# Optimization experiments

Measured on AMD Instinct MI355X. Metric: run time of the kernel, lower is better.

## Reference

```python
import jax, jax.numpy as jnp
import numpy as np
from jax import lax

B, N, D, L, EDGE_H, NGNN = 8, 128, 256, 64, 64, 3


def setup_inputs() -> dict:
    key = jax.random.key(0)
    ks = iter(jax.random.split(key, 64))
    def nrm(shape, s=0.02):
        return jax.random.normal(next(ks), shape, jnp.float32) * s
    inp = {}
    inp["node_feats"] = jax.random.uniform(next(ks), (B, N, 11), jnp.float32)
    inp["edge_feats"] = jax.random.normal(next(ks), (B, N, N, 3), jnp.float32)
    inp["adj_mask"] = jax.random.randint(next(ks), (B, N, N), 0, 2).astype(bool)
    inp["layer_costs"] = jax.random.uniform(next(ks), (B, L), jnp.float32)
    inp["global_dynamic"] = jax.random.uniform(next(ks), (B, 2), jnp.float32)
    inp["p_node_w"] = nrm((11, D)); inp["p_node_b"] = jnp.zeros((D,), jnp.float32)
    inp["g_w1"] = nrm((NGNN, D + 3, EDGE_H)); inp["g_b1"] = jnp.zeros((NGNN, EDGE_H), jnp.float32)
    inp["g_w2"] = nrm((NGNN, EDGE_H, D)); inp["g_b2"] = jnp.zeros((NGNN, D), jnp.float32)
    inp["u_w1"] = nrm((NGNN, 3 * D, D)); inp["u_b1"] = jnp.zeros((NGNN, D), jnp.float32)
    inp["u_w2"] = nrm((NGNN, D, D)); inp["u_b2"] = jnp.zeros((NGNN, D), jnp.float32)
    inp["ln_g"] = jnp.ones((NGNN, D), jnp.float32); inp["ln_b"] = jnp.zeros((NGNN, D), jnp.float32)
    inp["conv_w"] = nrm((32, 1, 4)); inp["conv_b"] = jnp.zeros((32,), jnp.float32)
    inp["lp_w"] = nrm((32 * 31, D)); inp["lp_b"] = jnp.zeros((D,), jnp.float32)
    inp["q_w"] = nrm((2 * D + 2, D)); inp["q_b"] = jnp.zeros((D,), jnp.float32)
    inp["k_w"] = nrm((D, D)); inp["k_b"] = jnp.zeros((D,), jnp.float32)
    inp["s_w1"] = nrm((D + 2, D)); inp["s_b1"] = jnp.zeros((D,), jnp.float32)
    inp["s_w2"] = nrm((D, 1)); inp["s_b2"] = jnp.zeros((1,), jnp.float32)
    inp["v_w1"] = nrm((2 * D + 2, D)); inp["v_b1"] = jnp.zeros((D,), jnp.float32)
    inp["v_w2"] = nrm((D, 1)); inp["v_b2"] = jnp.zeros((1,), jnp.float32)
    return inp


def _ecgc(h, edge_feats, adj_bool, gw1, gb1, gw2, gb2, uw1, ub1, uw2, ub2, lng, lnb):
    Bh, Nn, Dd = h.shape
    # h_j: features of sender node j broadcast over receiver axis -> (B, N, N, D)
    h_j = jnp.broadcast_to(h[:, None, :, :], (Bh, Nn, Nn, Dd))
    gate_in = jnp.concatenate([h_j, edge_feats], axis=-1)            # (B,N,N,D+3)
    gates = jax.nn.sigmoid(jax.nn.relu(gate_in @ gw1 + gb1) @ gw2 + gb2)
    msg = gates * h_j                                                # (B,N,N,D)
    m = adj_bool.astype(h.dtype)[..., None]
    cnt = jnp.maximum(m.sum(axis=2), 1.0)                            # (B,N,1)
    agg_mean = (msg * m).sum(axis=2) / cnt                           # (B,N,D)
    agg_max = jnp.where(adj_bool[..., None], msg, -jnp.inf).max(axis=2)
    agg_max = jnp.where(jnp.isinf(agg_max), 0.0, agg_max)
    ui = jnp.concatenate([h, agg_mean, agg_max], axis=-1)            # (B,N,3D)
    x = h + (jax.nn.relu(ui @ uw1 + ub1) @ uw2 + ub2)
    mu = x.mean(-1, keepdims=True)
    var = ((x - mu) ** 2).mean(-1, keepdims=True)
    return (x - mu) * lax.rsqrt(var + 1e-5) * lng + lnb


def reference(node_feats, edge_feats, adj_mask, layer_costs, global_dynamic,
              p_node_w, p_node_b, g_w1, g_b1, g_w2, g_b2, u_w1, u_b1, u_w2, u_b2,
              ln_g, ln_b, conv_w, conv_b, lp_w, lp_b, q_w, q_b, k_w, k_b,
              s_w1, s_b1, s_w2, s_b2, v_w1, v_b1, v_w2, v_b2):
    # layer cost encoder: Conv1d(1,32,k=4,s=2) + ReLU, flatten, Linear
    le = lax.conv_general_dilated(layer_costs[:, None, :], conv_w, (2,), 'VALID',
                                  dimension_numbers=('NCH', 'OIH', 'NCH'))
    le = jax.nn.relu(le + conv_b[None, :, None])                     # (B,32,31)
    layer_embed = le.reshape(le.shape[0], -1) @ lp_w + lp_b          # (B,D)
    h = node_feats @ p_node_w + p_node_b                             # (B,N,D)
    for i in range(g_w1.shape[0]):
        h = _ecgc(h, edge_feats, adj_mask, g_w1[i], g_b1[i], g_w2[i], g_b2[i],
                  u_w1[i], u_b1[i], u_w2[i], u_b2[i], ln_g[i], ln_b[i])
    w = (node_feats[:, :, 0] * node_feats[:, :, 7])[..., None]       # (B,N,1)
    graph_embed = (w * h).sum(axis=1) / jnp.maximum(w.sum(axis=1), 1e-8)
    qi = jnp.concatenate([graph_embed, layer_embed, global_dynamic], axis=-1)
    query = qi @ q_w + q_b                                           # (B,D)
    keys = h @ k_w + k_b                                             # (B,N,D)
    device_scores = jnp.einsum('bnd,bd->bn', keys, query) / jnp.sqrt(jnp.float32(query.shape[-1]))
    si = jnp.concatenate([graph_embed, global_dynamic], axis=-1)
    stop_logit = jax.nn.relu(si @ s_w1 + s_b1) @ s_w2 + s_b2         # (B,1)
    all_logits = jnp.concatenate([device_scores, stop_logit], axis=1)
    value = jax.nn.relu(qi @ v_w1 + v_b1) @ v_w2 + v_b2              # (B,1)
    return all_logits, value, h
```

## Files before the change

### kernel.cpp

```cpp
#include <hip/hip_runtime.h>
#include <hip/hip_bf16.h>
#include <math.h>

#define BB 8
#define NN_ 128
#define DD 256
#define LL 64
#define EH 64
#define NG 3

typedef __attribute__((ext_vector_type(8))) short bs8;
typedef __attribute__((ext_vector_type(4))) float f4;

__device__ __forceinline__ short f2bf(float f) {
    __hip_bfloat16 h = __float2bfloat16(f);
    return *reinterpret_cast<short*>(&h);
}

__device__ __forceinline__ bs8 cvt8(const float* __restrict__ p) {
    bs8 r;
    #pragma unroll
    for (int i = 0; i < 8; ++i) r[i] = f2bf(p[i]);
    return r;
}

__device__ __forceinline__ float blockReduceSum(float v, float* sRed) {
    int tid = threadIdx.x;
    __syncthreads();
    sRed[tid] = v;
    __syncthreads();
    for (int s = 128; s > 0; s >>= 1) {
        if (tid < s) sRed[tid] += sRed[tid + s];
        __syncthreads();
    }
    return sRed[0];
}

__global__ __launch_bounds__(256) void k_prep(
    const float* __restrict__ uw1, const float* __restrict__ uw2,
    const float* __restrict__ gw2, const float* __restrict__ gw1,
    const float* __restrict__ kw, const unsigned char* __restrict__ adj,
    const float* __restrict__ lc, const float* __restrict__ cw,
    const float* __restrict__ cb, const float* __restrict__ lpw,
    const float* __restrict__ nf, const float* __restrict__ pnw,
    const float* __restrict__ pnb, const float* __restrict__ gb1,
    unsigned short* __restrict__ w1t, unsigned short* __restrict__ w2t,
    unsigned short* __restrict__ g2t, unsigned short* __restrict__ g1t,
    unsigned short* __restrict__ kwt, int* __restrict__ mode,
    float* __restrict__ lpart, float* __restrict__ wsum,
    float* __restrict__ h, float* __restrict__ preg)
{
    const int blk = blockIdx.x, tid = threadIdx.x;
    if (blk == 232) {
        __shared__ int sOff, sBig;
        __shared__ float sRedD[256];
        if (tid == 0) { sOff = 0; sBig = 0; }
        __syncthreads();
        int off = 0, big = 0;
        #pragma unroll
        for (int k = 0; k < 4; ++k) {
            unsigned char v = adj[tid * 4 + k];
            if (v > 1) big = 1;
            if (k != 0 && v != 0) off = 1;
        }
        if (off) atomicOr(&sOff, 1);
        if (big) atomicOr(&sBig, 1);
        __syncthreads();
        if (tid == 0) mode[0] = sBig ? 2 : (sOff ? 0 : 1);
        for (int bb = 0; bb < 8; ++bb) {
            float v = 0.f;
            if (tid < 128) {
                const float* p = nf + (size_t)(bb * 128 + tid) * 11;
                v = p[0] * p[7];
            }
            float s = blockReduceSum(v, sRedD);
            if (tid == 0) wsum[bb] = s;
        }
        return;
    }
    if (blk >= 489) {
        const int row0 = (blk - 489) * 16;
        __shared__ float sF[16][12];
        __shared__ float sCW[12][64];
        if (tid < 176) sF[tid / 11][tid % 11] = nf[(size_t)(row0 + tid / 11) * 11 + tid % 11];
        {
            const int t = tid & 63, f0 = tid >> 6;
            const float* r0p = pnw + (size_t)f0 * DD;
            const float* r1p = pnw + (size_t)(f0 + 4) * DD;
            const float* r2p = (f0 + 8 < 11) ? (pnw + (size_t)(f0 + 8) * DD) : pnb;
            float a0 = 0.f, a1 = 0.f, a2 = 0.f;
            for (int k = 0; k < 256; ++k) {
                float g = gw1[k * EH + t];
                a0 += r0p[k] * g; a1 += r1p[k] * g; a2 += r2p[k] * g;
            }
            if (f0 + 8 == 11) a2 += gb1[t];
            sCW[f0][t] = a0; sCW[f0 + 4][t] = a1; sCW[f0 + 8][t] = a2;
        }
        __syncthreads();
        float acc[16];
        {
            float bb = pnb[tid];
            #pragma unroll
            for (int rr = 0; rr < 16; ++rr) acc[rr] = bb;
        }
        #pragma unroll
        for (int f = 0; f < 11; ++f) {
            float wf = pnw[f * DD + tid];
            #pragma unroll
            for (int rr = 0; rr < 16; ++rr) acc[rr] += sF[rr][f] * wf;
        }
        #pragma unroll
        for (int rr = 0; rr < 16; ++rr)
            h[(size_t)(row0 + rr) * DD + tid] = acc[rr];
        {
            const int t = tid & 63, r0 = tid >> 6;
            #pragma unroll
            for (int q = 0; q < 4; ++q) {
                int rr = r0 * 4 + q;
                float a = sCW[11][t];
                #pragma unroll
                for (int f = 0; f < 11; ++f) a += sF[rr][f] * sCW[f][t];
                preg[(size_t)(row0 + rr) * EH + t] = a;
            }
        }
        return;
    }
    if (blk > 232) {
        const int lb = blk - 233;
        const int b = lb >> 5, kseg = (lb >> 2) & 7, c4 = lb & 3;
        const int d = tid & 63, ss = tid >> 6;
        __shared__ float sC[LL];
        __shared__ float sV[124];
        __shared__ float sP[4][64];
        if (tid < LL) sC[tid] = lc[b * LL + tid];
        __syncthreads();
        if (tid < 124) {
            int idx = kseg * 124 + tid;
            int c = idx / 31, t = idx - c * 31;
            float a = cb[c];
            #pragma unroll
            for (int k = 0; k < 4; ++k) a += sC[2 * t + k] * cw[c * 4 + k];
            sV[tid] = fmaxf(a, 0.f);
        }
        __syncthreads();
        float acc = 0.f;
        for (int k = ss; k < 124; k += 4)
            acc += sV[k] * lpw[(size_t)(kseg * 124 + k) * DD + c4 * 64 + d];
        sP[ss][d] = acc;
        __syncthreads();
        if (ss == 0)
            lpart[(b * 32 + kseg * 4 + c4) * 64 + d] = sP[0][d] + sP[1][d] + sP[2][d] + sP[3][d];
        return;
    }
    const float* src; unsigned short* dst; int K, kt, dt, srcw = 256;
    if (blk < 144)      { int l = blk / 48, t = blk % 48; kt = t >> 2; dt = t & 3;
                          src = uw1 + (size_t)l * 196608; dst = w1t + (size_t)l * 196608; K = 768; }
    else if (blk < 192) { int x = blk - 144, l = x / 16, t = x % 16; kt = t >> 2; dt = t & 3;
                          src = uw2 + (size_t)l * 65536; dst = w2t + (size_t)l * 65536; K = 256; }
    else if (blk < 204) { int x = blk - 192, l = x >> 2; kt = 0; dt = x & 3;
                          src = gw2 + (size_t)l * 16384; dst = g2t + (size_t)l * 16384; K = 64; }
    else if (blk < 216) { int x = blk - 204, l = x >> 2; kt = x & 3; dt = 0; srcw = 64;
                          src = gw1 + (size_t)l * 16576; dst = g1t + (size_t)l * 16384; K = 256; }
    else                { int x = blk - 216; kt = x >> 2; dt = x & 3;
                          src = kw; dst = kwt; K = 256; }
    __shared__ float sT[64][65];
    #pragma unroll
    for (int q = 0; q < 16; ++q) {
        int idx = q * 256 + tid, kk = idx >> 6, dd = idx & 63;
        sT[kk][dd] = src[(size_t)(kt * 64 + kk) * srcw + dt * 64 + dd];
    }
    __syncthreads();
    const int d = tid >> 2, kc = (tid & 3) * 16;
    unsigned short* drow = dst + (size_t)(dt * 64 + d) * K + kt * 64 + kc;
    #pragma unroll
    for (int i = 0; i < 16; ++i) drow[i] = (unsigned short)f2bf(sT[kc + i][d]);
}

__global__ __launch_bounds__(256) void k_edge(
    const float* __restrict__ h, const float* __restrict__ preg,
    const float* __restrict__ edge, const void* __restrict__ adj,
    const int* __restrict__ mode,
    const float* __restrict__ gw1,
    const unsigned short* __restrict__ g2t,
    const float* __restrict__ gb2,
    float* __restrict__ agg_mean, float* __restrict__ agg_max)
{
    const int tid = threadIdx.x;
    const int bi = blockIdx.x;
    const int b = bi >> 7;
    const int lane = tid & 63, w = tid >> 6;
    const int lrow = lane >> 4, lcol = lane & 15;
    const int md = mode[0];

    __shared__ __align__(16) unsigned int sHid[4096];
    __shared__ float sWe[192];
    __shared__ float sE[384];
    __shared__ unsigned long long sMask[2];

    if (tid < 192) sWe[tid] = gw1[16384 + tid];
    const float* eB = edge + (size_t)bi * 384;
    for (int idx = tid; idx < 384; idx += 256) sE[idx] = eB[idx];
    if (tid < 128) {
        int mv;
        if (md == 1)      mv = ((const int*)adj)[(size_t)bi * NN_ + tid] != 0;
        else if (md == 2) mv = ((const float*)adj)[(size_t)bi * NN_ + tid] != 0.f;
        else              mv = ((const unsigned char*)adj)[(size_t)bi * NN_ + tid] != 0;
        unsigned long long bal = __ballot(mv);
        if ((tid & 63) == 0) sMask[tid >> 6] = bal;
    }
    __syncthreads();

    const float* pB = preg + (size_t)b * NN_ * EH;
    #pragma unroll
    for (int q = 0; q < 16; ++q) {
        int idx = q * 256 + tid;
        int j = idx >> 5, p = idx & 31;
        float2 pv = *(const float2*)(pB + j * EH + 2 * p);
        float e0 = sE[j * 3], e1 = sE[j * 3 + 1], e2 = sE[j * 3 + 2];
        int t0 = 2 * p, t1 = t0 + 1;
        float v0 = fmaxf(pv.x + e0 * sWe[t0] + e1 * sWe[64 + t0] + e2 * sWe[128 + t0], 0.f);
        float v1 = fmaxf(pv.y + e0 * sWe[t1] + e1 * sWe[64 + t1] + e2 * sWe[128 + t1], 0.f);
        unsigned int pk = (unsigned int)(unsigned short)f2bf(v0) |
                          ((unsigned int)(unsigned short)f2bf(v1) << 16);
        sHid[j * 32 + (p ^ ((j & 7) << 2))] = pk;
    }
    __syncthreads();

    const unsigned long long m0 = sMask[0], m1 = sMask[1];
    const float cntf = (float)(__popcll(m0) + __popcll(m1));

    bs8 bfr[4][2];
    float bg[4];
    #pragma unroll
    for (int nt = 0; nt < 4; ++nt) {
        int d = w * 64 + nt * 16 + lcol;
        bg[nt] = gb2[d];
        #pragma unroll
        for (int ks = 0; ks < 2; ++ks) {
            int k0 = ks * 32 + lrow * 8;
            bfr[nt][ks] = *(const bs8*)(g2t + (size_t)d * 64 + k0);
        }
    }

    const float* hB = h + (size_t)b * NN_ * DD;
    float vs[4] = {0.f, 0.f, 0.f, 0.f};
    float vm[4] = {-INFINITY, -INFINITY, -INFINITY, -INFINITY};

    #pragma unroll
    for (int pp = 0; pp < 2; ++pp) {
        f4 acc[4][4] = {};
        #pragma unroll
        for (int ks = 0; ks < 2; ++ks) {
            bs8 afr[4];
            #pragma unroll
            for (int m = 0; m < 4; ++m) {
                int j = pp * 64 + m * 16 + lcol;
                int k0 = ks * 32 + lrow * 8;
                afr[m] = *(const bs8*)(sHid + (j * 32 + ((k0 >> 1) ^ ((j & 7) << 2))));
            }
            #pragma unroll
            for (int m = 0; m < 4; ++m)
                #pragma unroll
                for (int nt = 0; nt < 4; ++nt)
                    acc[m][nt] = __builtin_amdgcn_mfma_f32_16x16x32_bf16(
                        afr[m], bfr[nt][ks], acc[m][nt], 0, 0, 0);
        }
        const unsigned long long mw = pp ? m1 : m0;
        #pragma unroll
        for (int m = 0; m < 4; ++m) {
            #pragma unroll
            for (int nt = 0; nt < 4; ++nt) {
                int dnt = w * 64 + nt * 16 + lcol;
                #pragma unroll
                for (int r = 0; r < 4; ++r) {
                    int bit = m * 16 + lrow * 4 + r;
                    float x = acc[m][nt][r] + bg[nt];
                    float g = __builtin_amdgcn_rcpf(1.0f + __expf(-x));
                    float msg = g * hB[(pp * 64 + bit) * DD + dnt];
                    int on = (int)((mw >> bit) & 1ULL);
                    vs[nt] += on ? msg : 0.f;
                    vm[nt] = fmaxf(vm[nt], on ? msg : -INFINITY);
                }
            }
        }
    }

    #pragma unroll
    for (int nt = 0; nt < 4; ++nt) {
        float s = vs[nt];
        s += __shfl_xor(s, 16); s += __shfl_xor(s, 32);
        vs[nt] = s;
        float m = vm[nt];
        m = fmaxf(m, __shfl_xor(m, 16)); m = fmaxf(m, __shfl_xor(m, 32));
        vm[nt] = m;
    }
    const int g = lrow;
    float ssel = (g == 0) ? vs[0] : (g == 1) ? vs[1] : (g == 2) ? vs[2] : vs[3];
    float msel = (g == 0) ? vm[0] : (g == 1) ? vm[1] : (g == 2) ? vm[2] : vm[3];
    const int d = w * 64 + lane;
    agg_mean[(size_t)bi * DD + d] = ssel / fmaxf(cntf, 1.f);
    agg_max[(size_t)bi * DD + d] = (cntf > 0.f) ? msel : 0.f;
}

__global__ __launch_bounds__(256) void k_updp(
    const float* __restrict__ h, const float* __restrict__ amean,
    const float* __restrict__ amax, const float* __restrict__ nf,
    const unsigned short* __restrict__ w1t,
    const float* __restrict__ ub1,
    const unsigned short* __restrict__ w2t,
    const float* __restrict__ ub2,
    const float* __restrict__ lng, const float* __restrict__ lnb,
    float* __restrict__ hout, float* __restrict__ out2,
    const unsigned short* __restrict__ g1tn, const float* __restrict__ gb1n,
    float* __restrict__ preg, float* __restrict__ gpart)
{
    const int tid = threadIdx.x;
    const int row0 = blockIdx.x * 4;
    const int lane = tid & 63, w = tid >> 6;
    const int lcol = lane & 15, lrow = lane >> 4;

    __shared__ __align__(16) unsigned int sX32[16 * 384];
    __shared__ __align__(16) unsigned short sH16[16 * 256];
    __shared__ float sRes[4][256];
    __shared__ float sOut[4][260];
    __shared__ float sWr[4];

    if (tid < 4) {
        const float* p = nf + (size_t)(row0 + tid) * 11;
        sWr[tid] = p[0] * p[7];
    }
    {
        const int j = w;
        const float* hR = h + (size_t)(row0 + j) * DD;
        const float* mR = amean + (size_t)(row0 + j) * DD;
        const float* xR = amax + (size_t)(row0 + j) * DD;
        #pragma unroll
        for (int q = 0; q < 6; ++q) {
            int p = lane + q * 64;
            int k = 2 * p;
            float2 v;
            if (k < 256)      { v = *(const float2*)(hR + k); sRes[j][k] = v.x; sRes[j][k + 1] = v.y; }
            else if (k < 512)   v = *(const float2*)(mR + (k - 256));
            else                v = *(const float2*)(xR + (k - 512));
            unsigned int pk = (unsigned int)(unsigned short)f2bf(v.x) |
                              ((unsigned int)(unsigned short)f2bf(v.y) << 16);
            sX32[j * 384 + (p ^ (j << 2))] = pk;
        }
    }
    __syncthreads();

    const char* sXb = (const char*)sX32;
    const unsigned short* w1r = w1t + (size_t)(w * 64 + lcol) * 768;
    f4 a0 = {0.f, 0.f, 0.f, 0.f}, a1 = a0, a2 = a0, a3 = a0;
    #pragma unroll 4
    for (int ks = 0; ks < 24; ++ks) {
        int k0 = ks * 32 + lrow * 8;
        bs8 av = *(const bs8*)(sXb + lcol * 1536 + ((((k0 >> 3) ^ (lcol & 7))) << 4));
        bs8 b0 = *(const bs8*)(w1r + k0);
        bs8 b1 = *(const bs8*)(w1r + 16 * 768 + k0);
        bs8 b2 = *(const bs8*)(w1r + 32 * 768 + k0);
        bs8 b3 = *(const bs8*)(w1r + 48 * 768 + k0);
        a0 = __builtin_amdgcn_mfma_f32_16x16x32_bf16(av, b0, a0, 0, 0, 0);
        a1 = __builtin_amdgcn_mfma_f32_16x16x32_bf16(av, b1, a1, 0, 0, 0);
        a2 = __builtin_amdgcn_mfma_f32_16x16x32_bf16(av, b2, a2, 0, 0, 0);
        a3 = __builtin_amdgcn_mfma_f32_16x16x32_bf16(av, b3, a3, 0, 0, 0);
    }
    if (lrow == 0) {
        #pragma unroll
        for (int nt = 0; nt < 4; ++nt) {
            int d = w * 64 + nt * 16 + lcol;
            float bb = ub1[d];
            f4 A = (nt == 0) ? a0 : (nt == 1) ? a1 : (nt == 2) ? a2 : a3;
            #pragma unroll
            for (int r = 0; r < 4; ++r) {
                float hv = fmaxf(A[r] + bb, 0.f);
                sH16[r * 256 + (d ^ (r << 3))] = (unsigned short)f2bf(hv);
            }
        }
    }
    __syncthreads();

    const unsigned short* w2r = w2t + (size_t)(w * 64 + lcol) * 256;
    f4 c0 = {0.f, 0.f, 0.f, 0.f}, c1 = c0, c2 = c0, c3 = c0;
    #pragma unroll
    for (int ks = 0; ks < 8; ++ks) {
        int k0 = ks * 32 + lrow * 8;
        bs8 av = *(const bs8*)((const char*)sH16 + lcol * 512 + ((((k0 >> 3) ^ (lcol & 7))) << 4));
        bs8 b0 = *(const bs8*)(w2r + k0);
        bs8 b1 = *(const bs8*)(w2r + 16 * 256 + k0);
        bs8 b2 = *(const bs8*)(w2r + 32 * 256 + k0);
        bs8 b3 = *(const bs8*)(w2r + 48 * 256 + k0);
        c0 = __builtin_amdgcn_mfma_f32_16x16x32_bf16(av, b0, c0, 0, 0, 0);
        c1 = __builtin_amdgcn_mfma_f32_16x16x32_bf16(av, b1, c1, 0, 0, 0);
        c2 = __builtin_amdgcn_mfma_f32_16x16x32_bf16(av, b2, c2, 0, 0, 0);
        c3 = __builtin_amdgcn_mfma_f32_16x16x32_bf16(av, b3, c3, 0, 0, 0);
    }
    if (lrow == 0) {
        #pragma unroll
        for (int nt = 0; nt < 4; ++nt) {
            int d = w * 64 + nt * 16 + lcol;
            float bb = ub2[d];
            f4 C = (nt == 0) ? c0 : (nt == 1) ? c1 : (nt == 2) ? c2 : c3;
            #pragma unroll
            for (int r = 0; r < 4; ++r)
                sOut[r][d] = C[r] + bb + sRes[r][d];
        }
    }
    __syncthreads();

    float xv[4], s = 0.f;
    #pragma unroll
    for (int q = 0; q < 4; ++q) { xv[q] = sOut[w][lane + 64 * q]; s += xv[q]; }
    #pragma unroll
    for (int off = 1; off < 64; off <<= 1) s += __shfl_xor(s, off);
    const float mu = s * (1.f / DD);
    float s2 = 0.f;
    #pragma unroll
    for (int q = 0; q < 4; ++q) { float d = xv[q] - mu; s2 += d * d; }
    #pragma unroll
    for (int off = 1; off < 64; off <<= 1) s2 += __shfl_xor(s2, off);
    const float inv = rsqrtf(s2 * (1.f / DD) + 1e-5f);
    #pragma unroll
    for (int q = 0; q < 4; ++q) {
        int c = lane + 64 * q;
        float res = (xv[q] - mu) * inv * lng[c] + lnb[c];
        hout[(size_t)(row0 + w) * DD + c] = res;
        if (out2) out2[(size_t)(row0 + w) * DD + c] = res;
        sOut[w][c] = res;
    }
    __syncthreads();
    if (g1tn) {
        const unsigned short* bR = g1tn + (size_t)(w * 16 + lcol) * 256;
        f4 p = {0.f, 0.f, 0.f, 0.f};
        #pragma unroll
        for (int ks = 0; ks < 8; ++ks) {
            int k0 = ks * 32 + lrow * 8;
            bs8 av = cvt8(&sOut[lcol & 3][k0]);
            bs8 bv = *(const bs8*)(bR + k0);
            p = __builtin_amdgcn_mfma_f32_16x16x32_bf16(av, bv, p, 0, 0, 0);
        }
        if (lrow == 0) {
            const float gb_ = gb1n[w * 16 + lcol];
            #pragma unroll
            for (int r = 0; r < 4; ++r)
                preg[(size_t)(row0 + r) * EH + w * 16 + lcol] = p[r] + gb_;
        }
    } else {
        float g = sWr[0] * sOut[0][tid] + sWr[1] * sOut[1][tid] +
                  sWr[2] * sOut[2][tid] + sWr[3] * sOut[3][tid];
        gpart[(size_t)blockIdx.x * DD + tid] = g;
    }
}

__global__ __launch_bounds__(256) void k_hmm(
    const float* __restrict__ gpart, const float* __restrict__ wsum,
    const float* __restrict__ gd,
    const float* __restrict__ qw, const float* __restrict__ sw1,
    const float* __restrict__ vw1,
    const float* __restrict__ lpb, const float* __restrict__ lpart,
    float* __restrict__ part)
{
    const int blk = blockIdx.x;
    const int m = blk >> 5, kseg = (blk >> 2) & 7, c4 = blk & 3;
    const int tid = threadIdx.x;
    const int d = tid & 63, ks = tid >> 6;
    const int K = (m == 1) ? 258 : 514;
    const int kc = (m == 1) ? 33 : 65;
    const int k0 = kseg * kc;
    const int klen = min(k0 + kc, K) - k0;
    __shared__ float sX[8 * 66];
    __shared__ float sP[4][8][64];
    for (int idx = tid; idx < 8 * kc; idx += 256) {
        int bb = idx / kc, kk = idx % kc, k = k0 + kk;
        float v = 0.f;
        if (k < K) {
            if (k < 256) {
                float s = 0.f;
                #pragma unroll 8
                for (int t = 0; t < 32; ++t)
                    s += gpart[(size_t)(bb * 32 + t) * DD + k];
                v = s / fmaxf(wsum[bb], 1e-8f);
            } else if (m == 1) {
                v = gd[bb * 2 + (k - 256)];
            } else if (k < 512) {
                int e = k - 256;
                v = lpb[e];
                #pragma unroll
                for (int s = 0; s < 8; ++s)
                    v += lpart[(bb * 32 + s * 4 + (e >> 6)) * 64 + (e & 63)];
            } else {
                v = gd[bb * 2 + (k - 512)];
            }
        }
        sX[bb * 66 + kk] = v;
    }
    __syncthreads();
    const float* W = (m == 0) ? qw : (m == 1) ? sw1 : vw1;
    const int dg = c4 * 64 + d;
    float acc[8] = {0.f, 0.f, 0.f, 0.f, 0.f, 0.f, 0.f, 0.f};
    for (int kk = ks; kk < klen; kk += 4) {
        float wv = W[(size_t)(k0 + kk) * DD + dg];
        #pragma unroll
        for (int bb = 0; bb < 8; ++bb) acc[bb] += sX[bb * 66 + kk] * wv;
    }
    #pragma unroll
    for (int bb = 0; bb < 8; ++bb) sP[ks][bb][d] = acc[bb];
    __syncthreads();
    for (int idx = tid; idx < 8 * 64; idx += 256) {
        int bb = idx >> 6, dd = idx & 63;
        float sum = sP[0][bb][dd] + sP[1][bb][dd] + sP[2][bb][dd] + sP[3][bb][dd];
        part[((m * 8 + kseg) * 8 + bb) * DD + c4 * 64 + dd] = sum;
    }
}

__global__ __launch_bounds__(256) void k_scr(
    const float* __restrict__ h, const unsigned short* __restrict__ kwt,
    const float* __restrict__ kb, const float* __restrict__ hpart,
    const float* __restrict__ qb,
    const float* __restrict__ sb1, const float* __restrict__ vb1,
    const float* __restrict__ sw2, const float* __restrict__ sb2,
    const float* __restrict__ vw2, const float* __restrict__ vb2,
    float* __restrict__ out)
{
    const int tid = threadIdx.x, blk = blockIdx.x;
    const int row0 = blk * 16, b = blk >> 3, chunk = blk & 7;
    const int lane = tid & 63, w = tid >> 6;
    const int lcol = lane & 15, lrow = lane >> 4;
    __shared__ float sQ[256];
    __shared__ float sPart[4][16];
    __shared__ float sRed[256];
    {
        float qv = qb[tid];
        #pragma unroll
        for (int kseg = 0; kseg < 8; ++kseg)
            qv += hpart[(size_t)(kseg * 8 + b) * DD + tid];
        sQ[tid] = qv;
    }
    __syncthreads();
    const float* aR = h + (size_t)(row0 + lcol) * DD;
    f4 acc[4] = {};
    #pragma unroll
    for (int ks = 0; ks < 8; ++ks) {
        int k0 = ks * 32 + lrow * 8;
        bs8 av = cvt8(aR + k0);
        #pragma unroll
        for (int nt = 0; nt < 4; ++nt) {
            bs8 bv = *(const bs8*)(kwt + (size_t)(w * 64 + nt * 16 + lcol) * 256 + k0);
            acc[nt] = __builtin_amdgcn_mfma_f32_16x16x32_bf16(av, bv, acc[nt], 0, 0, 0);
        }
    }
    float part[4] = {0.f, 0.f, 0.f, 0.f};
    #pragma unroll
    for (int nt = 0; nt < 4; ++nt) {
        int col = w * 64 + nt * 16 + lcol;
        float q = sQ[col], kv = kb[col];
        #pragma unroll
        for (int r = 0; r < 4; ++r) part[r] += (acc[nt][r] + kv) * q;
    }
    #pragma unroll
    for (int r = 0; r < 4; ++r) {
        float s = part[r];
        s += __shfl_xor(s, 1); s += __shfl_xor(s, 2);
        s += __shfl_xor(s, 4); s += __shfl_xor(s, 8);
        part[r] = s;
    }
    if (lcol == 0) {
        #pragma unroll
        for (int r = 0; r < 4; ++r) sPart[w][lrow * 4 + r] = part[r];
    }
    __syncthreads();
    if (tid < 16) {
        float s = sPart[0][tid] + sPart[1][tid] + sPart[2][tid] + sPart[3][tid];
        out[b * 129 + (row0 & (NN_ - 1)) + tid] = s * 0.0625f;
    }
    if (chunk == 0) {
        float s = sb1[tid], v = vb1[tid];
        #pragma unroll
        for (int kseg = 0; kseg < 8; ++kseg) {
            s += hpart[(size_t)((8 + kseg) * 8 + b) * DD + tid];
            v += hpart[(size_t)((16 + kseg) * 8 + b) * DD + tid];
        }
        s = fmaxf(s, 0.f); v = fmaxf(v, 0.f);
        float stop = blockReduceSum(s * sw2[tid], sRed);
        float val  = blockReduceSum(v * vw2[tid], sRed);
        if (tid == 0) {
            out[b * 129 + 128] = stop + sb2[0];
            out[1032 + b] = val + vb2[0];
        }
    }
}

extern "C" void kernel_launch(void* const* d_in, const int* in_sizes, int n_in,
                              void* d_out, int out_size, void* d_ws, size_t ws_size,
                              hipStream_t stream) {
    (void)in_sizes; (void)n_in; (void)out_size; (void)ws_size;
    const float* nf  = (const float*)d_in[0];
    const float* ef  = (const float*)d_in[1];
    const void*  adj = d_in[2];
    const float* lc  = (const float*)d_in[3];
    const float* gd  = (const float*)d_in[4];
    const float* pnw = (const float*)d_in[5];
    const float* pnb = (const float*)d_in[6];
    const float* gw1 = (const float*)d_in[7];
    const float* gb1 = (const float*)d_in[8];
    const float* gw2 = (const float*)d_in[9];
    const float* gb2 = (const float*)d_in[10];
    const float* uw1 = (const float*)d_in[11];
    const float* ub1 = (const float*)d_in[12];
    const float* uw2 = (const float*)d_in[13];
    const float* ub2 = (const float*)d_in[14];
    const float* lng = (const float*)d_in[15];
    const float* lnb = (const float*)d_in[16];
    const float* cw  = (const float*)d_in[17];
    const float* cb  = (const float*)d_in[18];
    const float* lpw = (const float*)d_in[19];
    const float* lpb = (const float*)d_in[20];
    const float* qw  = (const float*)d_in[21];
    const float* qb  = (const float*)d_in[22];
    const float* kw  = (const float*)d_in[23];
    const float* kb  = (const float*)d_in[24];
    const float* sw1 = (const float*)d_in[25];
    const float* sb1 = (const float*)d_in[26];
    const float* sw2 = (const float*)d_in[27];
    const float* sb2 = (const float*)d_in[28];
    const float* vw1 = (const float*)d_in[29];
    const float* vb1 = (const float*)d_in[30];
    const float* vw2 = (const float*)d_in[31];
    const float* vb2 = (const float*)d_in[32];

    float* ws = (float*)d_ws;
    float* h     = ws;
    float* preg  = ws + 262144;
    float* amean = ws + 327680;
    float* amax  = ws + 589824;
    float* lpart = ws + 851968;
    float* hpart = ws + 868352;
    float* gpart = ws + 917504;
    float* wsum  = ws + 983040;
    int*   mode  = (int*)(ws + 983048);
    unsigned short* uw1t = (unsigned short*)(ws + 983052);
    unsigned short* uw2t = (unsigned short*)(ws + 1277964);
    unsigned short* g2t  = (unsigned short*)(ws + 1376268);
    unsigned short* g1t  = (unsigned short*)(ws + 1400844);
    unsigned short* kwt  = (unsigned short*)(ws + 1425420);
    float* out   = (float*)d_out;

    k_prep<<<553, 256, 0, stream>>>(uw1, uw2, gw2, gw1, kw,
                                    (const unsigned char*)adj,
                                    lc, cw, cb, lpw, nf, pnw, pnb, gb1,
                                    uw1t, uw2t, g2t, g1t, kwt, mode, lpart, wsum,
                                    h, preg);
    for (int i = 0; i < NG; ++i) {
        const float* gw1i = gw1 + (size_t)i * 259 * EH;
        float* out2sel = (i == NG - 1) ? (out + 1040) : (float*)nullptr;
        const unsigned short* g1tn = (i < NG - 1) ? (g1t + (size_t)(i + 1) * 16384)
                                                  : (const unsigned short*)nullptr;
        const float* gb1n = (i < NG - 1) ? (gb1 + (i + 1) * EH) : (const float*)nullptr;
        k_edge<<<BB * NN_, 256, 0, stream>>>(h, preg, ef, adj, mode, gw1i,
                                             g2t + (size_t)i * 16384,
                                             gb2 + i * DD, amean, amax);
        k_updp<<<BB * NN_ / 4, 256, 0, stream>>>(h, amean, amax, nf,
                                                 uw1t + (size_t)i * 196608, ub1 + i * DD,
                                                 uw2t + (size_t)i * 65536, ub2 + i * DD,
                                                 lng + i * DD, lnb + i * DD, h, out2sel,
                                                 g1tn, gb1n, preg, gpart);
    }
    k_hmm<<<96, 256, 0, stream>>>(gpart, wsum, gd, qw, sw1, vw1, lpb, lpart, hpart);
    k_scr<<<BB * NN_ / 16, 256, 0, stream>>>(h, kwt, kb, hpart, qb, sb1, vb1,
                                             sw2, sb2, vw2, vb2, out);
}
```

Before: 186.0 us.

## Fuse edge aggregation and node update into one per-layer kernel

Merges the per-receiver edge-gating/aggregation kernel and the update MLP kernel into a single k_layer kernel. Each block handles four receiver rows, double-buffering the bf16 hidden tile in shared memory and keeping the mean/max aggregates in LDS instead of writing them to global memory. h and preg are ping-ponged between two buffers so that in-place updates stay safe across blocks. This removes one launch per layer and the global round-trip of the aggregates. In exchange the grid shrinks from 1024 to 256 blocks, per-block shared memory grows, and each block now runs its four edge rows serially, which may reduce parallelism.

```diff
diff --git a/kernel.cpp b/kernel.cpp
--- a/kernel.cpp
+++ b/kernel.cpp
@@ -176,59 +176,55 @@
     for (int i = 0; i < 16; ++i) drow[i] = (unsigned short)f2bf(sT[kc + i][d]);
 }
 
-__global__ __launch_bounds__(256) void k_edge(
-    const float* __restrict__ h, const float* __restrict__ preg,
-    const float* __restrict__ edge, const void* __restrict__ adj,
-    const int* __restrict__ mode,
-    const float* __restrict__ gw1,
-    const unsigned short* __restrict__ g2t,
-    const float* __restrict__ gb2,
-    float* __restrict__ agg_mean, float* __restrict__ agg_max)
+__global__ __launch_bounds__(256) void k_layer(
+    const float* __restrict__ hin, float* __restrict__ hout,
+    const float* __restrict__ pin, float* __restrict__ pout,
+    const float* __restrict__ ef, const void* __restrict__ adj,
+    const int* __restrict__ mode, const float* __restrict__ gw1We,
+    const unsigned short* __restrict__ g2t, const float* __restrict__ gb2,
+    const unsigned short* __restrict__ w1t, const float* __restrict__ ub1,
+    const unsigned short* __restrict__ w2t, const float* __restrict__ ub2,
+    const float* __restrict__ lng, const float* __restrict__ lnb,
+    const float* __restrict__ nf, float* __restrict__ out2,
+    const unsigned short* __restrict__ g1tn, const float* __restrict__ gb1n,
+    float* __restrict__ gpart)
 {
-    const int tid = threadIdx.x;
-    const int bi = blockIdx.x;
-    const int b = bi >> 7;
+    const int tid = threadIdx.x, bid = blockIdx.x;
+    const int row0 = bid * 4, b = row0 >> 7;
     const int lane = tid & 63, w = tid >> 6;
-    const int lrow = lane >> 4, lcol = lane & 15;
+    const int lcol = lane & 15, lrow = lane >> 4;
     const int md = mode[0];
 
-    __shared__ __align__(16) unsigned int sHid[4096];
+    __shared__ __align__(16) char uA[32768];
+    __shared__ float aggM[4][256], aggX[4][256];
+    __shared__ float sRes[4][256];
+    __shared__ float sOut[4][260];
     __shared__ float sWe[192];
-    __shared__ float sE[384];
-    __shared__ unsigned long long sMask[2];
-
-    if (tid < 192) sWe[tid] = gw1[16384 + tid];
-    const float* eB = edge + (size_t)bi * 384;
-    for (int idx = tid; idx < 384; idx += 256) sE[idx] = eB[idx];
-    if (tid < 128) {
-        int mv;
-        if (md == 1)      mv = ((const int*)adj)[(size_t)bi * NN_ + tid] != 0;
-        else if (md == 2) mv = ((const float*)adj)[(size_t)bi * NN_ + tid] != 0.f;
-        else              mv = ((const unsigned char*)adj)[(size_t)bi * NN_ + tid] != 0;
-        unsigned long long bal = __ballot(mv);
-        if ((tid & 63) == 0) sMask[tid >> 6] = bal;
-    }
-    __syncthreads();
-
-    const float* pB = preg + (size_t)b * NN_ * EH;
-    #pragma unroll
-    for (int q = 0; q < 16; ++q) {
-        int idx = q * 256 + tid;
-        int j = idx >> 5, p = idx & 31;
-        float2 pv = *(const float2*)(pB + j * EH + 2 * p);
-        float e0 = sE[j * 3], e1 = sE[j * 3 + 1], e2 = sE[j * 3 + 2];
-        int t0 = 2 * p, t1 = t0 + 1;
-        float v0 = fmaxf(pv.x + e0 * sWe[t0] + e1 * sWe[64 + t0] + e2 * sWe[128 + t0], 0.f);
-        float v1 = fmaxf(pv.y + e0 * sWe[t1] + e1 * sWe[64 + t1] + e2 * sWe[128 + t1], 0.f);
-        unsigned int pk = (unsigned int)(unsigned short)f2bf(v0) |
-                          ((unsigned int)(unsigned short)f2bf(v1) << 16);
-        sHid[j * 32 + (p ^ ((j & 7) << 2))] = pk;
-    }
-    __syncthreads();
-
-    const unsigned long long m0 = sMask[0], m1 = sMask[1];
-    const float cntf = (float)(__popcll(m0) + __popcll(m1));
-
+    __shared__ float sE[4][384];
+    __shared__ unsigned long long sMask[4][2];
+    __shared__ float sWr[4];
+
+    if (tid < 192) sWe[tid] = gw1We[tid];
+    for (int idx = tid; idx < 4 * 384; idx += 256) {
+        int n = idx / 384, e = idx - n * 384;
+        sE[n][e] = ef[(size_t)(row0 + n) * 384 + e];
+    }
+    #pragma unroll
+    for (int n = 0; n < 4; ++n) {
+        if (tid < 128) {
+            size_t ai = (size_t)(row0 + n) * NN_ + tid;
+            int mv;
+            if (md == 1)      mv = ((const int*)adj)[ai] != 0;
+            else if (md == 2) mv = ((const float*)adj)[ai] != 0.f;
+            else              mv = ((const unsigned char*)adj)[ai] != 0;
+            unsigned long long bal = __ballot(mv);
+            if ((tid & 63) == 0) sMask[n][tid >> 6] = bal;
+        }
+    }
+    if (tid < 4) {
+        const float* p = nf + (size_t)(row0 + tid) * 11;
+        sWr[tid] = p[0] * p[7];
+    }
     bs8 bfr[4][2];
     float bg[4];
     #pragma unroll
@@ -236,114 +232,118 @@
         int d = w * 64 + nt * 16 + lcol;
         bg[nt] = gb2[d];
         #pragma unroll
-        for (int ks = 0; ks < 2; ++ks) {
-            int k0 = ks * 32 + lrow * 8;
-            bfr[nt][ks] = *(const bs8*)(g2t + (size_t)d * 64 + k0);
-        }
-    }
-
-    const float* hB = h + (size_t)b * NN_ * DD;
-    float vs[4] = {0.f, 0.f, 0.f, 0.f};
-    float vm[4] = {-INFINITY, -INFINITY, -INFINITY, -INFINITY};
-
-    #pragma unroll
-    for (int pp = 0; pp < 2; ++pp) {
-        f4 acc[4][4] = {};
-        #pragma unroll
-        for (int ks = 0; ks < 2; ++ks) {
-            bs8 afr[4];
-            #pragma unroll
-            for (int m = 0; m < 4; ++m) {
-                int j = pp * 64 + m * 16 + lcol;
-                int k0 = ks * 32 + lrow * 8;
-                afr[m] = *(const bs8*)(sHid + (j * 32 + ((k0 >> 1) ^ ((j & 7) << 2))));
-            }
-            #pragma unroll
-            for (int m = 0; m < 4; ++m)
+        for (int ks = 0; ks < 2; ++ks)
+            bfr[nt][ks] = *(const bs8*)(g2t + (size_t)d * 64 + ks * 32 + lrow * 8);
+    }
+
+    const float* pB = pin + (size_t)b * NN_ * EH;
+    const float* hB = hin + (size_t)b * NN_ * DD;
+    unsigned int* const buf0 = (unsigned int*)uA;
+    unsigned int* const buf1 = (unsigned int*)(uA + 16384);
+
+    auto hidStage = [&](unsigned int* dst, int n) {
+        #pragma unroll
+        for (int q = 0; q < 16; ++q) {
+            int idx = q * 256 + tid;
+            int j = idx >> 5, p = idx & 31;
+            float2 pv = *(const float2*)(pB + j * EH + 2 * p);
+            float e0 = sE[n][j * 3], e1 = sE[n][j * 3 + 1], e2 = sE[n][j * 3 + 2];
+            int t0 = 2 * p, t1 = t0 + 1;
+            float v0 = fmaxf(pv.x + e0 * sWe[t0] + e1 * sWe[64 + t0] + e2 * sWe[128 + t0], 0.f);
+            float v1 = fmaxf(pv.y + e0 * sWe[t1] + e1 * sWe[64 + t1] + e2 * sWe[128 + t1], 0.f);
+            unsigned int pk = (unsigned int)(unsigned short)f2bf(v0) |
+                              ((unsigned int)(unsigned short)f2bf(v1) << 16);
+            dst[j * 32 + (p ^ ((j & 7) << 2))] = pk;
+        }
+    };
+
+    __syncthreads();
+    hidStage(buf0, 0);
+    __syncthreads();
+    int cur = 0;
+    #pragma unroll
+    for (int n = 0; n < 4; ++n) {
+        if (n < 3) hidStage(cur ? buf0 : buf1, n + 1);
+        {
+            const unsigned int* sHid = cur ? buf1 : buf0;
+            const unsigned long long m0 = sMask[n][0], m1 = sMask[n][1];
+            const float cntf = (float)(__popcll(m0) + __popcll(m1));
+            float vs[4] = {0.f, 0.f, 0.f, 0.f};
+            float vm[4] = {-INFINITY, -INFINITY, -INFINITY, -INFINITY};
+            #pragma unroll
+            for (int pp = 0; pp < 2; ++pp) {
+                f4 acc[4][4] = {};
                 #pragma unroll
-                for (int nt = 0; nt < 4; ++nt)
-                    acc[m][nt] = __builtin_amdgcn_mfma_f32_16x16x32_bf16(
-                        afr[m], bfr[nt][ks], acc[m][nt], 0, 0, 0);
-        }
-        const unsigned long long mw = pp ? m1 : m0;
-        #pragma unroll
-        for (int m = 0; m < 4; ++m) {
-            #pragma unroll
-            for (int nt = 0; nt < 4; ++nt) {
-                int dnt = w * 64 + nt * 16 + lcol;
+                for (int ks = 0; ks < 2; ++ks) {
+                    bs8 afr[4];
+                    #pragma unroll
+                    for (int m = 0; m < 4; ++m) {
+                        int j = pp * 64 + m * 16 + lcol;
+                        int k0 = ks * 32 + lrow * 8;
+                        afr[m] = *(const bs8*)(sHid + (j * 32 + ((k0 >> 1) ^ ((j & 7) << 2))));
+                    }
+                    #pragma unroll
+                    for (int m = 0; m < 4; ++m)
+                        #pragma unroll
+                        for (int nt = 0; nt < 4; ++nt)
+                            acc[m][nt] = __builtin_amdgcn_mfma_f32_16x16x32_bf16(
+                                afr[m], bfr[nt][ks], acc[m][nt], 0, 0, 0);
+                }
+                const unsigned long long mw = pp ? m1 : m0;
                 #pragma unroll
-                for (int r = 0; r < 4; ++r) {
-                    int bit = m * 16 + lrow * 4 + r;
-                    float x = acc[m][nt][r] + bg[nt];
-                    float g = __builtin_amdgcn_rcpf(1.0f + __expf(-x));
-                    float msg = g * hB[(pp * 64 + bit) * DD + dnt];
-                    int on = (int)((mw >> bit) & 1ULL);
-                    vs[nt] += on ? msg : 0.f;
-                    vm[nt] = fmaxf(vm[nt], on ? msg : -INFINITY);
+                for (int m = 0; m < 4; ++m) {
+                    #pragma unroll
+                    for (int nt = 0; nt < 4; ++nt) {
+                        int dnt = w * 64 + nt * 16 + lcol;
+                        #pragma unroll
+                        for (int r = 0; r < 4; ++r) {
+                            int bit = m * 16 + lrow * 4 + r;
+                            float x = acc[m][nt][r] + bg[nt];
+                            float g = __builtin_amdgcn_rcpf(1.0f + __expf(-x));
+                            float msg = g * hB[(pp * 64 + bit) * DD + dnt];
+                            int on = (int)((mw >> bit) & 1ULL);
+                            vs[nt] += on ? msg : 0.f;
+                            vm[nt] = fmaxf(vm[nt], on ? msg : -INFINITY);
+                        }
+                    }
                 }
             }
-        }
-    }
-
-    #pragma unroll
-    for (int nt = 0; nt < 4; ++nt) {
-        float s = vs[nt];
-        s += __shfl_xor(s, 16); s += __shfl_xor(s, 32);
-        vs[nt] = s;
-        float m = vm[nt];
-        m = fmaxf(m, __shfl_xor(m, 16)); m = fmaxf(m, __shfl_xor(m, 32));
-        vm[nt] = m;
-    }
-    const int g = lrow;
-    float ssel = (g == 0) ? vs[0] : (g == 1) ? vs[1] : (g == 2) ? vs[2] : vs[3];
-    float msel = (g == 0) ? vm[0] : (g == 1) ? vm[1] : (g == 2) ? vm[2] : vm[3];
-    const int d = w * 64 + lane;
-    agg_mean[(size_t)bi * DD + d] = ssel / fmaxf(cntf, 1.f);
-    agg_max[(size_t)bi * DD + d] = (cntf > 0.f) ? msel : 0.f;
-}
-
-__global__ __launch_bounds__(256) void k_updp(
-    const float* __restrict__ h, const float* __restrict__ amean,
-    const float* __restrict__ amax, const float* __restrict__ nf,
-    const unsigned short* __restrict__ w1t,
-    const float* __restrict__ ub1,
-    const unsigned short* __restrict__ w2t,
-    const float* __restrict__ ub2,
-    const float* __restrict__ lng, const float* __restrict__ lnb,
-    float* __restrict__ hout, float* __restrict__ out2,
-    const unsigned short* __restrict__ g1tn, const float* __restrict__ gb1n,
-    float* __restrict__ preg, float* __restrict__ gpart)
-{
-    const int tid = threadIdx.x;
-    const int row0 = blockIdx.x * 4;
-    const int lane = tid & 63, w = tid >> 6;
-    const int lcol = lane & 15, lrow = lane >> 4;
-
-    __shared__ __align__(16) unsigned int sX32[16 * 384];
-    __shared__ __align__(16) unsigned short sH16[16 * 256];
-    __shared__ float sRes[4][256];
-    __shared__ float sOut[4][260];
-    __shared__ float sWr[4];
-
-    if (tid < 4) {
-        const float* p = nf + (size_t)(row0 + tid) * 11;
-        sWr[tid] = p[0] * p[7];
-    }
+            #pragma unroll
+            for (int nt = 0; nt < 4; ++nt) {
+                float s = vs[nt];
+                s += __shfl_xor(s, 16); s += __shfl_xor(s, 32);
+                vs[nt] = s;
+                float m = vm[nt];
+                m = fmaxf(m, __shfl_xor(m, 16)); m = fmaxf(m, __shfl_xor(m, 32));
+                vm[nt] = m;
+            }
+            const int g = lrow;
+            float ssel = (g == 0) ? vs[0] : (g == 1) ? vs[1] : (g == 2) ? vs[2] : vs[3];
+            float msel = (g == 0) ? vm[0] : (g == 1) ? vm[1] : (g == 2) ? vm[2] : vm[3];
+            const int d = w * 64 + lane;
+            aggM[n][d] = ssel / fmaxf(cntf, 1.f);
+            aggX[n][d] = (cntf > 0.f) ? msel : 0.f;
+        }
+        cur ^= 1;
+        __syncthreads();
+    }
+
+    unsigned int* sX32 = (unsigned int*)uA;
+    unsigned short* sH16 = (unsigned short*)(uA + 24576);
     {
         const int j = w;
-        const float* hR = h + (size_t)(row0 + j) * DD;
-        const float* mR = amean + (size_t)(row0 + j) * DD;
-        const float* xR = amax + (size_t)(row0 + j) * DD;
+        const float* hR = hin + (size_t)(row0 + j) * DD;
         #pragma unroll
         for (int q = 0; q < 6; ++q) {
             int p = lane + q * 64;
             int k = 2 * p;
-            float2 v;
-            if (k < 256)      { v = *(const float2*)(hR + k); sRes[j][k] = v.x; sRes[j][k + 1] = v.y; }
-            else if (k < 512)   v = *(const float2*)(mR + (k - 256));
-            else                v = *(const float2*)(xR + (k - 512));
-            unsigned int pk = (unsigned int)(unsigned short)f2bf(v.x) |
-                              ((unsigned int)(unsigned short)f2bf(v.y) << 16);
+            float v0, v1;
+            if (k < 256)      { float2 v = *(const float2*)(hR + k); v0 = v.x; v1 = v.y;
+                                sRes[j][k] = v0; sRes[j][k + 1] = v1; }
+            else if (k < 512) { v0 = aggM[j][k - 256]; v1 = aggM[j][k - 255]; }
+            else              { v0 = aggX[j][k - 512]; v1 = aggX[j][k - 511]; }
+            unsigned int pk = (unsigned int)(unsigned short)f2bf(v0) |
+                              ((unsigned int)(unsigned short)f2bf(v1) << 16);
             sX32[j * 384 + (p ^ (j << 2))] = pk;
         }
     }
@@ -443,12 +443,12 @@
             const float gb_ = gb1n[w * 16 + lcol];
             #pragma unroll
             for (int r = 0; r < 4; ++r)
-                preg[(size_t)(row0 + r) * EH + w * 16 + lcol] = p[r] + gb_;
+                pout[(size_t)(row0 + r) * EH + w * 16 + lcol] = p[r] + gb_;
         }
     } else {
         float g = sWr[0] * sOut[0][tid] + sWr[1] * sOut[1][tid] +
                   sWr[2] * sOut[2][tid] + sWr[3] * sOut[3][tid];
-        gpart[(size_t)blockIdx.x * DD + tid] = g;
+        gpart[(size_t)bid * DD + tid] = g;
     }
 }
 
@@ -629,43 +629,45 @@
     const float* vb2 = (const float*)d_in[32];
 
     float* ws = (float*)d_ws;
-    float* h     = ws;
-    float* preg  = ws + 262144;
-    float* amean = ws + 327680;
-    float* amax  = ws + 589824;
-    float* lpart = ws + 851968;
-    float* hpart = ws + 868352;
-    float* gpart = ws + 917504;
-    float* wsum  = ws + 983040;
-    int*   mode  = (int*)(ws + 983048);
-    unsigned short* uw1t = (unsigned short*)(ws + 983052);
-    unsigned short* uw2t = (unsigned short*)(ws + 1277964);
-    unsigned short* g2t  = (unsigned short*)(ws + 1376268);
-    unsigned short* g1t  = (unsigned short*)(ws + 1400844);
-    unsigned short* kwt  = (unsigned short*)(ws + 1425420);
+    float* h0    = ws;
+    float* h1    = ws + 262144;
+    float* pregA = ws + 524288;
+    float* pregB = ws + 589824;
+    float* lpart = ws + 655360;
+    float* hpart = ws + 671744;
+    float* gpart = ws + 720896;
+    float* wsum  = ws + 786432;
+    int*   mode  = (int*)(ws + 786440);
+    unsigned short* uw1t = (unsigned short*)(ws + 786444);
+    unsigned short* uw2t = (unsigned short*)(ws + 1081356);
+    unsigned short* g2t  = (unsigned short*)(ws + 1179660);
+    unsigned short* g1t  = (unsigned short*)(ws + 1204236);
+    unsigned short* kwt  = (unsigned short*)(ws + 1228812);
     float* out   = (float*)d_out;
 
     k_prep<<<553, 256, 0, stream>>>(uw1, uw2, gw2, gw1, kw,
                                     (const unsigned char*)adj,
                                     lc, cw, cb, lpw, nf, pnw, pnb, gb1,
                                     uw1t, uw2t, g2t, g1t, kwt, mode, lpart, wsum,
-                                    h, preg);
+                                    h0, pregA);
+    float* hin = h0;  float* hout = h1;
+    float* pin = pregA; float* pout = pregB;
     for (int i = 0; i < NG; ++i) {
-        const float* gw1i = gw1 + (size_t)i * 259 * EH;
         float* out2sel = (i == NG - 1) ? (out + 1040) : (float*)nullptr;
         const unsigned short* g1tn = (i < NG - 1) ? (g1t + (size_t)(i + 1) * 16384)
                                                   : (const unsigned short*)nullptr;
         const float* gb1n = (i < NG - 1) ? (gb1 + (i + 1) * EH) : (const float*)nullptr;
-        k_edge<<<BB * NN_, 256, 0, stream>>>(h, preg, ef, adj, mode, gw1i,
-                                             g2t + (size_t)i * 16384,
-                                             gb2 + i * DD, amean, amax);
-        k_updp<<<BB * NN_ / 4, 256, 0, stream>>>(h, amean, amax, nf,
-                                                 uw1t + (size_t)i * 196608, ub1 + i * DD,
-                                                 uw2t + (size_t)i * 65536, ub2 + i * DD,
-                                                 lng + i * DD, lnb + i * DD, h, out2sel,
-                                                 g1tn, gb1n, preg, gpart);
+        k_layer<<<BB * NN_ / 4, 256, 0, stream>>>(hin, hout, pin, pout, ef, adj, mode,
+                                                  gw1 + (size_t)i * 16576 + 16384,
+                                                  g2t + (size_t)i * 16384, gb2 + i * DD,
+                                                  uw1t + (size_t)i * 196608, ub1 + i * DD,
+                                                  uw2t + (size_t)i * 65536, ub2 + i * DD,
+                                                  lng + i * DD, lnb + i * DD, nf,
+                                                  out2sel, g1tn, gb1n, gpart);
+        float* t = hin; hin = hout; hout = t;
+        t = pin; pin = pout; pout = t;
     }
     k_hmm<<<96, 256, 0, stream>>>(gpart, wsum, gd, qw, sw1, vw1, lpb, lpart, hpart);
-    k_scr<<<BB * NN_ / 16, 256, 0, stream>>>(h, kwt, kb, hpart, qb, sb1, vb1,
+    k_scr<<<BB * NN_ / 16, 256, 0, stream>>>(hin, kwt, kb, hpart, qb, sb1, vb1,
                                              sw2, sb2, vw2, vb2, out);
 }
```

Measured after the change: 285.2 us. +53.3%, slower.

## Read sender features from a transposed bf16 copy in edge kernel

Applied to the files above, without the earlier changes.

Adds a transposed bf16 copy of the node features (hT, laid out [b][d][n]). It is written by the prep and update kernels, and the edge kernel reads it with 4-wide vector loads instead of strided fp32 gathers of h. The h and preg buffers are now double-buffered (ping-pong) across GNN layers so the update kernel no longer writes in place over inputs other blocks may still read. The cost is an extra scattered 2-byte store per element in the update kernel and reduced precision of the message operand.

```diff
diff --git a/kernel.cpp b/kernel.cpp
--- a/kernel.cpp
+++ b/kernel.cpp
@@ -11,10 +11,16 @@
 
 typedef __attribute__((ext_vector_type(8))) short bs8;
 typedef __attribute__((ext_vector_type(4))) float f4;
+typedef __attribute__((ext_vector_type(4))) unsigned short us4;
 
 __device__ __forceinline__ short f2bf(float f) {
     __hip_bfloat16 h = __float2bfloat16(f);
     return *reinterpret_cast<short*>(&h);
+}
+
+__device__ __forceinline__ float bf2f(unsigned short u) {
+    unsigned int x = ((unsigned int)u) << 16;
+    return __uint_as_float(x);
 }
 
 __device__ __forceinline__ bs8 cvt8(const float* __restrict__ p) {
@@ -48,7 +54,8 @@
     unsigned short* __restrict__ g2t, unsigned short* __restrict__ g1t,
     unsigned short* __restrict__ kwt, int* __restrict__ mode,
     float* __restrict__ lpart, float* __restrict__ wsum,
-    float* __restrict__ h, float* __restrict__ preg)
+    float* __restrict__ h, float* __restrict__ preg,
+    unsigned short* __restrict__ hT)
 {
     const int blk = blockIdx.x, tid = threadIdx.x;
     if (blk == 232) {
@@ -80,6 +87,7 @@
     }
     if (blk >= 489) {
         const int row0 = (blk - 489) * 16;
+        const int b = row0 >> 7, n0 = row0 & 127;
         __shared__ float sF[16][12];
         __shared__ float sCW[12][64];
         if (tid < 176) sF[tid / 11][tid % 11] = nf[(size_t)(row0 + tid / 11) * 11 + tid % 11];
@@ -109,9 +117,12 @@
             #pragma unroll
             for (int rr = 0; rr < 16; ++rr) acc[rr] += sF[rr][f] * wf;
         }
-        #pragma unroll
-        for (int rr = 0; rr < 16; ++rr)
+        unsigned short* hTb = hT + ((size_t)b * 256 + tid) * 128 + n0;
+        #pragma unroll
+        for (int rr = 0; rr < 16; ++rr) {
             h[(size_t)(row0 + rr) * DD + tid] = acc[rr];
+            hTb[rr] = (unsigned short)f2bf(acc[rr]);
+        }
         {
             const int t = tid & 63, r0 = tid >> 6;
             #pragma unroll
@@ -177,7 +188,7 @@
 }
 
 __global__ __launch_bounds__(256) void k_edge(
-    const float* __restrict__ h, const float* __restrict__ preg,
+    const unsigned short* __restrict__ hT, const float* __restrict__ preg,
     const float* __restrict__ edge, const void* __restrict__ adj,
     const int* __restrict__ mode,
     const float* __restrict__ gw1,
@@ -242,7 +253,7 @@
         }
     }
 
-    const float* hB = h + (size_t)b * NN_ * DD;
+    const unsigned short* hTb = hT + (size_t)b * 256 * 128;
     float vs[4] = {0.f, 0.f, 0.f, 0.f};
     float vm[4] = {-INFINITY, -INFINITY, -INFINITY, -INFINITY};
 
@@ -271,12 +282,13 @@
             #pragma unroll
             for (int nt = 0; nt < 4; ++nt) {
                 int dnt = w * 64 + nt * 16 + lcol;
+                us4 hv = *(const us4*)(hTb + (size_t)dnt * 128 + pp * 64 + m * 16 + lrow * 4);
                 #pragma unroll
                 for (int r = 0; r < 4; ++r) {
                     int bit = m * 16 + lrow * 4 + r;
                     float x = acc[m][nt][r] + bg[nt];
                     float g = __builtin_amdgcn_rcpf(1.0f + __expf(-x));
-                    float msg = g * hB[(pp * 64 + bit) * DD + dnt];
+                    float msg = g * bf2f(hv[r]);
                     int on = (int)((mw >> bit) & 1ULL);
                     vs[nt] += on ? msg : 0.f;
                     vm[nt] = fmaxf(vm[nt], on ? msg : -INFINITY);
@@ -312,12 +324,14 @@
     const float* __restrict__ lng, const float* __restrict__ lnb,
     float* __restrict__ hout, float* __restrict__ out2,
     const unsigned short* __restrict__ g1tn, const float* __restrict__ gb1n,
-    float* __restrict__ preg, float* __restrict__ gpart)
+    float* __restrict__ preg, float* __restrict__ gpart,
+    unsigned short* __restrict__ hT)
 {
     const int tid = threadIdx.x;
     const int row0 = blockIdx.x * 4;
     const int lane = tid & 63, w = tid >> 6;
     const int lcol = lane & 15, lrow = lane >> 4;
+    const int b = row0 >> 7, n0 = row0 & 127;
 
     __shared__ __align__(16) unsigned int sX32[16 * 384];
     __shared__ __align__(16) unsigned short sH16[16 * 256];
@@ -426,6 +440,7 @@
         float res = (xv[q] - mu) * inv * lng[c] + lnb[c];
         hout[(size_t)(row0 + w) * DD + c] = res;
         if (out2) out2[(size_t)(row0 + w) * DD + c] = res;
+        hT[((size_t)b * 256 + c) * 128 + n0 + w] = (unsigned short)f2bf(res);
         sOut[w][c] = res;
     }
     __syncthreads();
@@ -629,43 +644,50 @@
     const float* vb2 = (const float*)d_in[32];
 
     float* ws = (float*)d_ws;
-    float* h     = ws;
-    float* preg  = ws + 262144;
-    float* amean = ws + 327680;
-    float* amax  = ws + 589824;
-    float* lpart = ws + 851968;
-    float* hpart = ws + 868352;
-    float* gpart = ws + 917504;
-    float* wsum  = ws + 983040;
-    int*   mode  = (int*)(ws + 983048);
-    unsigned short* uw1t = (unsigned short*)(ws + 983052);
-    unsigned short* uw2t = (unsigned short*)(ws + 1277964);
-    unsigned short* g2t  = (unsigned short*)(ws + 1376268);
-    unsigned short* g1t  = (unsigned short*)(ws + 1400844);
-    unsigned short* kwt  = (unsigned short*)(ws + 1425420);
+    float* h0    = ws;
+    float* h1    = ws + 262144;
+    float* pregA = ws + 524288;
+    float* pregB = ws + 589824;
+    float* amean = ws + 655360;
+    float* amax  = ws + 917504;
+    float* lpart = ws + 1179648;
+    float* hpart = ws + 1196032;
+    float* gpart = ws + 1245184;
+    float* wsum  = ws + 1310720;
+    int*   mode  = (int*)(ws + 1310728);
+    unsigned short* uw1t = (unsigned short*)(ws + 1310732);
+    unsigned short* uw2t = (unsigned short*)(ws + 1605644);
+    unsigned short* g2t  = (unsigned short*)(ws + 1703948);
+    unsigned short* g1t  = (unsigned short*)(ws + 1728524);
+    unsigned short* kwt  = (unsigned short*)(ws + 1753100);
+    unsigned short* hT   = (unsigned short*)(ws + 1785868);
     float* out   = (float*)d_out;
 
     k_prep<<<553, 256, 0, stream>>>(uw1, uw2, gw2, gw1, kw,
                                     (const unsigned char*)adj,
                                     lc, cw, cb, lpw, nf, pnw, pnb, gb1,
                                     uw1t, uw2t, g2t, g1t, kwt, mode, lpart, wsum,
-                                    h, preg);
+                                    h0, pregA, hT);
+    float* hin = h0;  float* hout = h1;
+    float* pin = pregA; float* pout = pregB;
     for (int i = 0; i < NG; ++i) {
-        const float* gw1i = gw1 + (size_t)i * 259 * EH;
         float* out2sel = (i == NG - 1) ? (out + 1040) : (float*)nullptr;
         const unsigned short* g1tn = (i < NG - 1) ? (g1t + (size_t)(i + 1) * 16384)
                                                   : (const unsigned short*)nullptr;
         const float* gb1n = (i < NG - 1) ? (gb1 + (i + 1) * EH) : (const float*)nullptr;
-        k_edge<<<BB * NN_, 256, 0, stream>>>(h, preg, ef, adj, mode, gw1i,
-                                             g2t + (size_t)i * 16384,
-                                             gb2 + i * DD, amean, amax);
-        k_updp<<<BB * NN_ / 4, 256, 0, stream>>>(h, amean, amax, nf,
+        k_edge<<<BB * NN_, 256, 0, stream>>>(hT, pin, ef, adj, mode,
+                                             gw1 + (size_t)i * 16576,
+                                             g2t + (size_t)i * 16384, gb2 + i * DD,
+                                             amean, amax);
+        k_updp<<<BB * NN_ / 4, 256, 0, stream>>>(hin, amean, amax, nf,
                                                  uw1t + (size_t)i * 196608, ub1 + i * DD,
                                                  uw2t + (size_t)i * 65536, ub2 + i * DD,
-                                                 lng + i * DD, lnb + i * DD, h, out2sel,
-                                                 g1tn, gb1n, preg, gpart);
+                                                 lng + i * DD, lnb + i * DD, hout, out2sel,
+                                                 g1tn, gb1n, pout, gpart, hT);
+        float* t = hin; hin = hout; hout = t;
+        t = pin; pin = pout; pout = t;
     }
     k_hmm<<<96, 256, 0, stream>>>(gpart, wsum, gd, qw, sw1, vw1, lpb, lpart, hpart);
-    k_scr<<<BB * NN_ / 16, 256, 0, stream>>>(h, kwt, kb, hpart, qb, sb1, vb1,
+    k_scr<<<BB * NN_ / 16, 256, 0, stream>>>(hin, kwt, kb, hpart, qb, sb1, vb1,
                                              sw2, sb2, vw2, vb2, out);
 }
```

After: 196.8 us. 1.06x slower.
